# Kernel optimization log

Measured on AMD Instinct MI355X. Metric: run time of the kernel, lower is better.

## Reference

```python
import jax, jax.numpy as jnp
import numpy as np

F_CTX = 16          # ctx_future_context_size
CONV_STRENGTH = 0.5 # ctx_conv_strength
LN_EPS = 1e-5


def _layernorm(x, w, eps=LN_EPS):
    mu = jnp.mean(x, axis=-1, keepdims=True)
    var = jnp.var(x, axis=-1, keepdims=True)
    return (x - mu) / jnp.sqrt(var + eps) * w


def setup_inputs() -> dict:
    key = jax.random.key(0)
    B, S, D, V = 2, 512, 1024, 32000
    k0, k1, k2, k3 = jax.random.split(key, 4)
    emb_norm = jax.random.normal(k0, (B, S, D), jnp.float32)
    W_lm = jax.random.normal(k1, (V, D), jnp.float32) * 0.02
    W_ctx = jax.random.normal(k2, (V, D), jnp.float32) * 0.02
    ln_w = jnp.ones((D,), jnp.float32)
    # labels cover seq_len + F - 1 future tokens (required by the gather/view)
    y = jax.random.randint(k3, (B, S + F_CTX - 1), 0, V, dtype=jnp.int32)
    return {"emb_norm": emb_norm, "W_lm": W_lm, "W_ctx": W_ctx, "ln_w": ln_w, "y": y}


def reference(emb_norm, W_lm, W_ctx, ln_w, y):
    B, S, D = emb_norm.shape
    V = W_lm.shape[0]
    F = F_CTX

    logits = jnp.einsum('bsd,vd->bsv', emb_norm, W_lm)             # lm_head.output_proj
    c = jnp.einsum('bsd,vd->bsv', _layernorm(emb_norm, ln_w), W_ctx)  # context_head

    # y_context[b, s, v] = count of v among the F future tokens y[b, s:s+F]
    # (faithful to gather(indices) + one_hot(...).sum(-2), without the huge one-hot)
    win = jnp.arange(S)[:, None] + jnp.arange(F)[None, :]          # (S, F)
    y_win = y[:, win]                                              # (B, S, F)
    b_idx = jnp.arange(B)[:, None, None]
    s_idx = jnp.arange(S)[None, :, None]
    y_context = jnp.zeros((B, S, V), jnp.float32).at[b_idx, s_idx, y_win].add(1.0)

    # weighted BCE-with-logits (mean over all elements, per-element weight)
    w = 1.0 + 0.5 * jnp.any(y_context > 1.0, axis=0).astype(jnp.float32)   # (S, V)
    t = (y_context > 0.0).astype(jnp.float32)
    bce = jnp.maximum(c, 0.0) - c * t + jnp.log1p(jnp.exp(-jnp.abs(c)))
    context_loss = jnp.mean(w * bce)

    # causal exponential-decay window sum over the last F positions of c
    ed = jnp.exp(-CONV_STRENGTH * jnp.arange(F - 1, -1, -1, dtype=jnp.float32))
    ed = ed / ed.sum()
    c_pad = jnp.pad(c, ((0, 0), (F - 1, 0), (0, 0)))
    context = jnp.zeros_like(c)
    for j in range(F):  # fixed small window (16)
        context = context + ed[j] * c_pad[:, j:j + S, :]

    logits = logits + context

    # cross entropy vs y[:, :-F+1] == y[:, :S], ignore_index = -1
    tgt = y[:, :S]
    logp = jax.nn.log_softmax(logits, axis=-1)
    valid = (tgt >= 0)
    tgt_safe = jnp.where(valid, tgt, 0)
    nll = -jnp.take_along_axis(logp, tgt_safe[..., None].astype(jnp.int32), axis=-1)[..., 0]
    loss = jnp.sum(nll * valid.astype(nll.dtype)) / jnp.maximum(jnp.sum(valid.astype(jnp.float32)), 1.0)

    return logits, loss, context_loss
```

## Files before the change

kernel.cpp:

```cpp
#include <hip/hip_runtime.h>
#include <hip/hip_bf16.h>

typedef unsigned short u16;
typedef unsigned int u32;
typedef __bf16 bf16x8 __attribute__((ext_vector_type(8)));
typedef float f32x4 __attribute__((ext_vector_type(4)));

#define SDIM 512
#define BDIM 2
#define DDIM 1024
#define VDIM 32000
#define FCTX 16
#define NROWS (BDIM * SDIM)
#define YSTR (SDIM + FCTX - 1)
#define CONV_CHUNK 64

__device__ __forceinline__ u16 f2bf(float f) {
    u32 u = __float_as_uint(f);
    u += 0x7fffu + ((u >> 16) & 1u);
    return (u16)(u >> 16);
}

__device__ __forceinline__ void gload_lds16(const void* g, void* l) {
    __builtin_amdgcn_global_load_lds((const __attribute__((address_space(1))) void*)g,
                                     (__attribute__((address_space(3))) void*)l, 16, 0, 0);
}

__global__ __launch_bounds__(256) void prep_a_kernel(
    const float* __restrict__ emb, const float* __restrict__ lnw,
    u16* __restrict__ Alm, u16* __restrict__ Actx)
{
    int row = blockIdx.x;
    int t = threadIdx.x;
    const float4* x4 = (const float4*)(emb + (size_t)row * DDIM);
    float4 v = x4[t];
    float s1 = v.x + v.y + v.z + v.w;
    float s2 = v.x*v.x + v.y*v.y + v.z*v.z + v.w*v.w;
#pragma unroll
    for (int off = 32; off; off >>= 1) {
        s1 += __shfl_down(s1, off, 64);
        s2 += __shfl_down(s2, off, 64);
    }
    __shared__ float r1[4], r2[4];
    int lane = t & 63, wave = t >> 6;
    if (lane == 0) { r1[wave] = s1; r2[wave] = s2; }
    __syncthreads();
    s1 = r1[0] + r1[1] + r1[2] + r1[3];
    s2 = r2[0] + r2[1] + r2[2] + r2[3];
    float mean = s1 * (1.f / DDIM);
    float var = s2 * (1.f / DDIM) - mean * mean;
    float rstd = rsqrtf(var + 1e-5f);
    float4 w = ((const float4*)lnw)[t];
    ushort4 a, b;
    a.x = f2bf(v.x); a.y = f2bf(v.y); a.z = f2bf(v.z); a.w = f2bf(v.w);
    b.x = f2bf((v.x - mean) * rstd * w.x);
    b.y = f2bf((v.y - mean) * rstd * w.y);
    b.z = f2bf((v.z - mean) * rstd * w.z);
    b.w = f2bf((v.w - mean) * rstd * w.w);
    ((ushort4*)(Alm + (size_t)row * DDIM))[t] = a;
    ((ushort4*)(Actx + (size_t)row * DDIM))[t] = b;
}

__global__ __launch_bounds__(256) void cast_kernel(
    const float4* __restrict__ src, ushort4* __restrict__ dst)
{
    int i = blockIdx.x * 256 + threadIdx.x;
    float4 f = src[i];
    ushort4 o;
    o.x = f2bf(f.x); o.y = f2bf(f.y); o.z = f2bf(f.z); o.w = f2bf(f.w);
    dst[i] = o;
}

__global__ __launch_bounds__(256) void gemm_kernel(
    const u16* __restrict__ A0, const u16* __restrict__ B0, float* __restrict__ C0,
    const u16* __restrict__ A1, const u16* __restrict__ B1, float* __restrict__ C1)
{
    constexpr int K = DDIM, N = VDIM;
    const u16* A; const u16* Bw; float* C;
    if (blockIdx.z == 0) { A = A0; Bw = B0; C = C0; }
    else                 { A = A1; Bw = B1; C = C1; }

    __shared__ __align__(16) u16 sA[128 * 32];
    __shared__ __align__(16) u16 sB[128 * 32];

    int t = threadIdx.x;
    int lane = t & 63, wave = t >> 6;
    int bm = blockIdx.x, bn = blockIdx.y;

    const u16* gA = A + (size_t)(bm * 128 + (t >> 2)) * K + (t & 3) * 8;
    const u16* gB = Bw + (size_t)(bn * 128 + (t >> 2)) * K + (t & 3) * 8;
    u16* lA = sA + t * 8;
    u16* lB = sB + t * 8;

    f32x4 acc[4][4] = {};

    int wrow = (wave >> 1) * 64;
    int wcol = (wave & 1) * 64;
    const u16* fA = sA + (wrow + (lane & 15)) * 32 + (lane >> 4) * 8;
    const u16* fB = sB + (wcol + (lane & 15)) * 32 + (lane >> 4) * 8;

    for (int kt = 0; kt < K; kt += 32) {
        gload_lds16(gA,           lA);
        gload_lds16(gA + 64 * K,  lA + 2048);
        gload_lds16(gB,           lB);
        gload_lds16(gB + 64 * K,  lB + 2048);
        gA += 32; gB += 32;
        __syncthreads();
        bf16x8 af[4], bfr[4];
#pragma unroll
        for (int i = 0; i < 4; ++i) af[i] = *(const bf16x8*)(fA + i * 16 * 32);
#pragma unroll
        for (int j = 0; j < 4; ++j) bfr[j] = *(const bf16x8*)(fB + j * 16 * 32);
#pragma unroll
        for (int i = 0; i < 4; ++i)
#pragma unroll
            for (int j = 0; j < 4; ++j)
                acc[i][j] = __builtin_amdgcn_mfma_f32_16x16x32_bf16(af[i], bfr[j], acc[i][j], 0, 0, 0);
        __syncthreads();
    }

    int q = lane >> 4, lr = lane & 15;
    int row0 = bm * 128 + wrow + q * 4;
    int col0 = bn * 128 + wcol + lr;
#pragma unroll
    for (int i = 0; i < 4; ++i)
#pragma unroll
        for (int j = 0; j < 4; ++j) {
            float* cp = C + (size_t)(row0 + i * 16) * N + col0 + j * 16;
#pragma unroll
            for (int r = 0; r < 4; ++r) cp[(size_t)r * N] = acc[i][j][r];
        }
}

__global__ __launch_bounds__(256) void conv_kernel(
    const float* __restrict__ c, float* __restrict__ logits, float* __restrict__ acc)
{
    int v = blockIdx.x * 256 + threadIdx.x;
    int s0 = blockIdx.y * CONV_CHUNK;
    int b = blockIdx.z;

    float coef[FCTX];
    float Z = 0.f;
#pragma unroll
    for (int i = 0; i < FCTX; ++i) { coef[i] = expf(-0.5f * i); Z += coef[i]; }
    float invZ = 1.f / Z;
#pragma unroll
    for (int i = 0; i < FCTX; ++i) coef[i] *= invZ;

    float ring[FCTX];
#pragma unroll
    for (int i = 0; i < FCTX; ++i) ring[i] = 0.f;

    size_t base = ((size_t)b * SDIM) * VDIM + v;

    if (s0 > 0) {
#pragma unroll
        for (int i = 1; i < FCTX; ++i) {
            int s = s0 - FCTX + i;
            ring[i] = c[base + (size_t)s * VDIM];
        }
    }

    float sp = 0.f;
    for (int t16 = 0; t16 < CONV_CHUNK; t16 += FCTX) {
#pragma unroll
        for (int u = 0; u < FCTX; ++u) {
            size_t off = base + (size_t)(s0 + t16 + u) * VDIM;
            float cv = c[off];
            ring[u] = cv;
            float ctx = 0.f;
#pragma unroll
            for (int i = 0; i < FCTX; ++i) ctx += coef[i] * ring[(u - i) & (FCTX - 1)];
            logits[off] += ctx;
            sp += fmaxf(cv, 0.f) + log1pf(expf(-fabsf(cv)));
        }
    }
#pragma unroll
    for (int off = 32; off; off >>= 1) sp += __shfl_down(sp, off, 64);
    __shared__ float rs[4];
    int lane = threadIdx.x & 63, wave = threadIdx.x >> 6;
    if (lane == 0) rs[wave] = sp;
    __syncthreads();
    if (threadIdx.x == 0) atomicAdd(acc + 1, rs[0] + rs[1] + rs[2] + rs[3]);
}

__device__ __forceinline__ float softplus(float x) {
    return fmaxf(x, 0.f) + log1pf(expf(-fabsf(x)));
}

__global__ __launch_bounds__(256) void corr_kernel(
    const float* __restrict__ c, const int* __restrict__ y, float* __restrict__ acc)
{
    int sid = blockIdx.x * 256 + threadIdx.x;
    float corr = 0.f;
    if (sid < SDIM) {
        int tok[2 * FCTX];
        for (int i = 0; i < FCTX; ++i) {
            tok[i] = y[sid + i];
            tok[FCTX + i] = y[YSTR + sid + i];
        }
        for (int k = 0; k < 2 * FCTX; ++k) {
            int v = tok[k];
            bool seen = false;
            for (int j = 0; j < k; ++j) seen |= (tok[j] == v);
            if (seen) continue;
            int c0 = 0, c1 = 0;
            for (int i = 0; i < FCTX; ++i) {
                c0 += (tok[i] == v);
                c1 += (tok[FCTX + i] == v);
            }
            float w = ((c0 > 1) || (c1 > 1)) ? 1.5f : 1.0f;
            float cv0 = c[(size_t)sid * VDIM + v];
            float cv1 = c[(size_t)(SDIM + sid) * VDIM + v];
            if (w > 1.f) corr += 0.5f * (softplus(cv0) + softplus(cv1));
            if (c0 > 0) corr -= w * cv0;
            if (c1 > 0) corr -= w * cv1;
        }
    }
    atomicAdd(acc + 1, corr);
}

__global__ __launch_bounds__(256) void loss_kernel(
    const float* __restrict__ logits, const int* __restrict__ y, float* __restrict__ acc)
{
    int row = blockIdx.x;
    int t = threadIdx.x;
    const float* lp = logits + (size_t)row * VDIM;
    float m = -3.4e38f, sum = 0.f;
    for (int i = t; i < VDIM; i += 256) {
        float x = lp[i];
        float nm = fmaxf(m, x);
        sum = sum * expf(m - nm) + expf(x - nm);
        m = nm;
    }
#pragma unroll
    for (int off = 32; off; off >>= 1) {
        float om = __shfl_down(m, off, 64);
        float os = __shfl_down(sum, off, 64);
        float nm = fmaxf(m, om);
        sum = sum * expf(m - nm) + os * expf(om - nm);
        m = nm;
    }
    __shared__ float sm[4], ss[4];
    int lane = t & 63, wave = t >> 6;
    if (lane == 0) { sm[wave] = m; ss[wave] = sum; }
    __syncthreads();
    if (t == 0) {
        float M = sm[0], S = ss[0];
        for (int wv = 1; wv < 4; ++wv) {
            float nm = fmaxf(M, sm[wv]);
            S = S * expf(M - nm) + ss[wv] * expf(sm[wv] - nm);
            M = nm;
        }
        int b = row >> 9, s = row & 511;
        int tgt = y[b * YSTR + s];
        float xt = lp[tgt];
        atomicAdd(acc, -(xt - M - logf(S)));
    }
}

__global__ void finalize_kernel(const float* __restrict__ acc, float* __restrict__ out)
{
    out[(size_t)NROWS * VDIM]     = acc[0] * (1.f / (float)NROWS);
    out[(size_t)NROWS * VDIM + 1] = acc[1] * (1.f / ((float)NROWS * (float)VDIM));
}

extern "C" void kernel_launch(void* const* d_in, const int* in_sizes, int n_in,
                              void* d_out, int out_size, void* d_ws, size_t ws_size,
                              hipStream_t stream)
{
    const float* emb  = (const float*)d_in[0];
    const float* Wlm  = (const float*)d_in[1];
    const float* Wctx = (const float*)d_in[2];
    const float* lnw  = (const float*)d_in[3];
    const int*   y    = (const int*)d_in[4];
    float* out = (float*)d_out;

    char* ws = (char*)d_ws;
    const size_t A_BYTES = (size_t)NROWS * DDIM * 2;
    const size_t W_BYTES = (size_t)VDIM * DDIM * 2;
    const size_t C_BYTES = (size_t)NROWS * VDIM * 4;
    u16*   Alm   = (u16*)ws;
    u16*   Actx  = (u16*)(ws + A_BYTES);
    u16*   WlmB  = (u16*)(ws + 2 * A_BYTES);
    u16*   WctxB = (u16*)(ws + 2 * A_BYTES + W_BYTES);
    float* c     = (float*)(ws + 2 * A_BYTES + 2 * W_BYTES);
    float* acc   = (float*)(ws + 2 * A_BYTES + 2 * W_BYTES + C_BYTES);

    hipMemsetAsync(acc, 0, 2 * sizeof(float), stream);
    prep_a_kernel<<<NROWS, 256, 0, stream>>>(emb, lnw, Alm, Actx);
    cast_kernel<<<(VDIM * DDIM / 4) / 256, 256, 0, stream>>>((const float4*)Wlm,  (ushort4*)WlmB);
    cast_kernel<<<(VDIM * DDIM / 4) / 256, 256, 0, stream>>>((const float4*)Wctx, (ushort4*)WctxB);
    gemm_kernel<<<dim3(NROWS / 128, VDIM / 128, 2), 256, 0, stream>>>(Alm, WlmB, out, Actx, WctxB, c);
    conv_kernel<<<dim3(VDIM / 256, SDIM / CONV_CHUNK, BDIM), 256, 0, stream>>>(c, out, acc);
    corr_kernel<<<2, 256, 0, stream>>>(c, y, acc);
    loss_kernel<<<NROWS, 256, 0, stream>>>(out, y, acc);
    finalize_kernel<<<1, 1, 0, stream>>>(acc, out);
}
```

Measured before the change: 799.4 us.

## Rewrite GEMM with 256x256 tiles, double-buffered swizzled LDS and phased MFMA schedule

Replaces the 128x128, K=32 single-buffered GEMM with a 512-thread, 256x256-tile kernel that uses K=64 stages, double-buffered 128KB LDS with an XOR swizzle, and an 8-phase schedule that interleaves global-to-LDS loads with MFMA work under explicit waitcnt, barriers and setprio. It also remaps block ids so consecutive blocks are spread across XCDs. The aim is to hide global load latency, raise data reuse per tile and avoid LDS bank conflicts in the dominant GEMM. In exchange, the larger tile and accumulator count raise register and LDS pressure, and the hand-placed waits and barriers have to match the staging order exactly to stay correct.

```diff
diff --git a/kernel.cpp b/kernel.cpp
--- a/kernel.cpp
+++ b/kernel.cpp
@@ -71,59 +71,116 @@
     dst[i] = o;
 }
 
-__global__ __launch_bounds__(256) void gemm_kernel(
+
+__device__ __forceinline__ void stage_half(const u16* __restrict__ mat, int grow0, int gcol0,
+                                           char* lds_half, int t)
+{
+    int r0 = t >> 3;
+    int swz = ((t & 7) ^ (r0 & 7)) * 8;
+    const u16* g0 = mat + (size_t)(grow0 + r0) * DDIM + gcol0 + swz;
+    gload_lds16(g0, lds_half + t * 16);
+    gload_lds16(g0 + (size_t)64 * DDIM, lds_half + 8192 + t * 16);
+}
+
+#define MFMA16(a, b, c) __builtin_amdgcn_mfma_f32_16x16x32_bf16(a, b, c, 0, 0, 0)
+#define VM4 asm volatile("s_waitcnt vmcnt(4)" ::: "memory")
+#define VM0 asm volatile("s_waitcnt vmcnt(0)" ::: "memory")
+#define NOP ((void)0)
+
+#define PHASE(BB, Q, STG, VM) do {                                              \
+    bf16x8 a00, a01, a10, a11;                                                  \
+    if ((Q) == 0) {                                                             \
+        _Pragma("unroll")                                                       \
+        for (int j = 0; j < 4; ++j) {                                           \
+            bfr[2*j]   = *(const bf16x8*)(Bln + (BB)*65536 + j*2048 + axor0);   \
+            bfr[2*j+1] = *(const bf16x8*)(Bln + (BB)*65536 + j*2048 + axor1);   \
+        }                                                                       \
+    }                                                                           \
+    { const char* Ab = Aln + (BB)*65536 + (2*(Q))*2048;                         \
+      a00 = *(const bf16x8*)(Ab + axor0);                                       \
+      a01 = *(const bf16x8*)(Ab + axor1);                                       \
+      a10 = *(const bf16x8*)(Ab + 2048 + axor0);                                \
+      a11 = *(const bf16x8*)(Ab + 2048 + axor1); }                              \
+    STG; VM;                                                                    \
+    __builtin_amdgcn_s_barrier();                                               \
+    asm volatile("s_waitcnt lgkmcnt(0)" ::: "memory");                          \
+    __builtin_amdgcn_sched_barrier(0);                                          \
+    __builtin_amdgcn_s_setprio(1);                                              \
+    _Pragma("unroll")                                                           \
+    for (int j = 0; j < 4; ++j) {                                               \
+        acc[2*(Q)][j]   = MFMA16(a00, bfr[2*j],   acc[2*(Q)][j]);               \
+        acc[2*(Q)][j]   = MFMA16(a01, bfr[2*j+1], acc[2*(Q)][j]);               \
+        acc[2*(Q)+1][j] = MFMA16(a10, bfr[2*j],   acc[2*(Q)+1][j]);             \
+        acc[2*(Q)+1][j] = MFMA16(a11, bfr[2*j+1], acc[2*(Q)+1][j]);             \
+    }                                                                           \
+    __builtin_amdgcn_s_setprio(0);                                              \
+    __builtin_amdgcn_s_barrier();                                               \
+} while (0)
+
+#define STAGE_A(BB, H, KT) stage_half(Amat, bm256 + (H)*128, (KT)*64, ldsb + (BB)*65536 + (H)*16384, t)
+#define STAGE_B(BB, H, KT) stage_half(Bmat, bn256 + (H)*128, (KT)*64, ldsb + (BB)*65536 + 32768 + (H)*16384, t)
+
+__global__ __launch_bounds__(512, 2) void gemm_kernel(
     const u16* __restrict__ A0, const u16* __restrict__ B0, float* __restrict__ C0,
     const u16* __restrict__ A1, const u16* __restrict__ B1, float* __restrict__ C1)
 {
-    constexpr int K = DDIM, N = VDIM;
-    const u16* A; const u16* Bw; float* C;
-    if (blockIdx.z == 0) { A = A0; Bw = B0; C = C0; }
-    else                 { A = A1; Bw = B1; C = C1; }
-
-    __shared__ __align__(16) u16 sA[128 * 32];
-    __shared__ __align__(16) u16 sB[128 * 32];
+    constexpr int N = VDIM;
+    __shared__ __align__(16) char lds_s[131072];
+    char* ldsb = lds_s;
+
+    int bid = blockIdx.x;
+    int wg = (bid & 7) * 125 + (bid >> 3);
+    int z = (wg >= 500) ? 1 : 0;
+    int rem = wg - z * 500;
+    int bn = rem >> 2, bm = rem & 3;
+
+    const u16* Amat; const u16* Bmat; float* C;
+    if (z == 0) { Amat = A0; Bmat = B0; C = C0; }
+    else        { Amat = A1; Bmat = B1; C = C1; }
 
     int t = threadIdx.x;
     int lane = t & 63, wave = t >> 6;
-    int bm = blockIdx.x, bn = blockIdx.y;
-
-    const u16* gA = A + (size_t)(bm * 128 + (t >> 2)) * K + (t & 3) * 8;
-    const u16* gB = Bw + (size_t)(bn * 128 + (t >> 2)) * K + (t & 3) * 8;
-    u16* lA = sA + t * 8;
-    u16* lB = sB + t * 8;
-
-    f32x4 acc[4][4] = {};
-
-    int wrow = (wave >> 1) * 64;
-    int wcol = (wave & 1) * 64;
-    const u16* fA = sA + (wrow + (lane & 15)) * 32 + (lane >> 4) * 8;
-    const u16* fB = sB + (wcol + (lane & 15)) * 32 + (lane >> 4) * 8;
-
-    for (int kt = 0; kt < K; kt += 32) {
-        gload_lds16(gA,           lA);
-        gload_lds16(gA + 64 * K,  lA + 2048);
-        gload_lds16(gB,           lB);
-        gload_lds16(gB + 64 * K,  lB + 2048);
-        gA += 32; gB += 32;
-        __syncthreads();
-        bf16x8 af[4], bfr[4];
-#pragma unroll
-        for (int i = 0; i < 4; ++i) af[i] = *(const bf16x8*)(fA + i * 16 * 32);
-#pragma unroll
-        for (int j = 0; j < 4; ++j) bfr[j] = *(const bf16x8*)(fB + j * 16 * 32);
-#pragma unroll
-        for (int i = 0; i < 4; ++i)
-#pragma unroll
-            for (int j = 0; j < 4; ++j)
-                acc[i][j] = __builtin_amdgcn_mfma_f32_16x16x32_bf16(af[i], bfr[j], acc[i][j], 0, 0, 0);
-        __syncthreads();
-    }
-
-    int q = lane >> 4, lr = lane & 15;
-    int row0 = bm * 128 + wrow + q * 4;
-    int col0 = bn * 128 + wcol + lr;
-#pragma unroll
-    for (int i = 0; i < 4; ++i)
+    int wr = wave >> 2, wc = wave & 3;
+    int l15 = lane & 15, lg = lane >> 4, l7 = lane & 7;
+    int bm256 = bm * 256, bn256 = bn * 256;
+
+    int axor0 = (lg * 16) ^ (l7 << 4);
+    int axor1 = (64 + lg * 16) ^ (l7 << 4);
+    const char* Aln = ldsb + wr * 16384 + l15 * 128;
+    const char* Bln = ldsb + 32768 + (wc >> 1) * 16384 + ((wc & 1) * 64 + l15) * 128;
+
+    f32x4 acc[8][4] = {};
+    bf16x8 bfr[8];
+
+    STAGE_A(0, 0, 0); STAGE_A(0, 1, 0); STAGE_B(0, 0, 0); STAGE_B(0, 1, 0);
+    STAGE_B(1, 0, 1); STAGE_B(1, 1, 1);
+    VM4;
+    __builtin_amdgcn_s_barrier();
+
+    for (int m = 0; m < 7; ++m) {
+        int k1 = 2 * m + 1, k2 = 2 * m + 2, k3 = 2 * m + 3;
+        PHASE(0, 0, STAGE_A(1, 0, k1), NOP);
+        PHASE(0, 1, STAGE_A(1, 1, k1), NOP);
+        PHASE(0, 2, STAGE_B(0, 0, k2), NOP);
+        PHASE(0, 3, STAGE_B(0, 1, k2), VM4);
+        PHASE(1, 0, STAGE_A(0, 0, k2), NOP);
+        PHASE(1, 1, STAGE_A(0, 1, k2), NOP);
+        PHASE(1, 2, STAGE_B(1, 0, k3), NOP);
+        PHASE(1, 3, STAGE_B(1, 1, k3), VM4);
+    }
+    PHASE(0, 0, STAGE_A(1, 0, 15), NOP);
+    PHASE(0, 1, STAGE_A(1, 1, 15), NOP);
+    PHASE(0, 2, NOP, NOP);
+    PHASE(0, 3, NOP, VM0);
+    PHASE(1, 0, NOP, NOP);
+    PHASE(1, 1, NOP, NOP);
+    PHASE(1, 2, NOP, NOP);
+    PHASE(1, 3, NOP, NOP);
+
+    int row0 = bm256 + wr * 128 + lg * 4;
+    int col0 = bn256 + wc * 64 + l15;
+#pragma unroll
+    for (int i = 0; i < 8; ++i)
 #pragma unroll
         for (int j = 0; j < 4; ++j) {
             float* cp = C + (size_t)(row0 + i * 16) * N + col0 + j * 16;
@@ -291,7 +348,7 @@
     prep_a_kernel<<<NROWS, 256, 0, stream>>>(emb, lnw, Alm, Actx);
     cast_kernel<<<(VDIM * DDIM / 4) / 256, 256, 0, stream>>>((const float4*)Wlm,  (ushort4*)WlmB);
     cast_kernel<<<(VDIM * DDIM / 4) / 256, 256, 0, stream>>>((const float4*)Wctx, (ushort4*)WctxB);
-    gemm_kernel<<<dim3(NROWS / 128, VDIM / 128, 2), 256, 0, stream>>>(Alm, WlmB, out, Actx, WctxB, c);
+    gemm_kernel<<<1000, 512, 0, stream>>>(Alm, WlmB, out, Actx, WctxB, c);
     conv_kernel<<<dim3(VDIM / 256, SDIM / CONV_CHUNK, BDIM), 256, 0, stream>>>(c, out, acc);
     corr_kernel<<<2, 256, 0, stream>>>(c, y, acc);
     loss_kernel<<<NROWS, 256, 0, stream>>>(out, y, acc);
```

Result: faster. 688.0 us (-13.9%).
